# Kernel optimization log

Measured on AMD Instinct MI355X. Metric: run time of the kernel, lower is better.

Reference implementation:

```python
import jax, jax.numpy as jnp
import numpy as np

WIRES = 4
KS = 2
STRIDE = 2
OUT_CH = 4
LAYERS = 4
N_ROT = 8
SEED = 42
RATIO_IMPRIM = 0.3  # pennylane RandomLayers default


def _build_structure():
    # Mimics pennylane.templates.RandomLayers with a fixed seed: per layer, draw
    # random single-qubit rotations (RX/RY/RZ on random wires, consuming weights)
    # interleaved with random CNOTs at ratio_imprim.
    rng = np.random.RandomState(SEED)
    gates = []
    for l in range(LAYERS):
        i = 0
        while i < N_ROT:
            if rng.random_sample() > RATIO_IMPRIM:
                g = int(rng.randint(3))  # 0:RX 1:RY 2:RZ
                w = int(rng.randint(WIRES))
                gates.append(("R", g, w, l, i))
                i += 1
            else:
                cw, tw = rng.choice(WIRES, 2, replace=False)
                gates.append(("CNOT", int(cw), int(tw), 0, 0))
    return gates

GATES = _build_structure()


def _apply_1q(state, U, wire):
    # state: [P,2,2,2,2]; U: [2,2] shared or [P,2,2] per-patch
    ax = wire + 1
    s = jnp.moveaxis(state, ax, -1)
    if U.ndim == 2:
        s = jnp.einsum('ab,...b->...a', U, s)
    else:
        s = jnp.einsum('pab,p...b->p...a', U, s)
    return jnp.moveaxis(s, -1, ax)


def _apply_cnot(state, control, target):
    c_ax, t_ax = control + 1, target + 1
    s0 = jax.lax.index_in_dim(state, 0, c_ax, keepdims=False)
    s1 = jax.lax.index_in_dim(state, 1, c_ax, keepdims=False)
    t2 = t_ax - 1 if t_ax > c_ax else t_ax  # target axis after removing control axis
    return jnp.stack([s0, jnp.flip(s1, axis=t2)], axis=c_ax)


def _rot(g, t):
    h = t * 0.5
    c = jnp.cos(h)
    s = jnp.sin(h)
    z = jnp.zeros_like(c)
    if g == 0:    # RX
        U = jnp.stack([jnp.stack([c + 0j, -1j * s]), jnp.stack([-1j * s, c + 0j])])
    elif g == 1:  # RY
        U = jnp.stack([jnp.stack([c + 0j, -s + 0j]), jnp.stack([s + 0j, c + 0j])])
    else:         # RZ
        U = jnp.stack([jnp.stack([c - 1j * s, z + 0j]), jnp.stack([z + 0j, c + 1j * s])])
    return U.astype(jnp.complex64)


def _circuit(angles, weights):
    # angles: [P,4] RY encoding angles; returns [P, OUT_CH] PauliZ expvals
    P = angles.shape[0]
    state = jnp.zeros((P,) + (2,) * WIRES, jnp.complex64)
    state = state.at[(slice(None),) + (0,) * WIRES].set(1.0)
    for j in range(KS * KS):  # data-encoding RY, per-patch angle
        h = angles[:, j] * 0.5
        c, s = jnp.cos(h), jnp.sin(h)
        U = jnp.stack([jnp.stack([c, -s], -1), jnp.stack([s, c], -1)], -2).astype(jnp.complex64)
        state = _apply_1q(state, U, j)
    for kind, a, b, l, i in GATES:
        if kind == "R":
            state = _apply_1q(state, _rot(a, weights[l, i]), b)
        else:
            state = _apply_cnot(state, a, b)
    probs = (state.real ** 2 + state.imag ** 2).reshape(P, 2 ** WIRES)
    idx = np.arange(2 ** WIRES)
    signs = np.stack([1.0 - 2.0 * ((idx >> (WIRES - 1 - j)) & 1) for j in range(OUT_CH)])
    return probs @ jnp.asarray(signs, jnp.float32).T


def setup_inputs() -> dict:
    key = jax.random.key(0)
    k1, k2 = jax.random.split(key)
    img = jax.random.uniform(k1, (32, 512, 512, 3), dtype=jnp.float32)
    weights = jax.random.uniform(k2, (LAYERS, N_ROT), dtype=jnp.float32) * (2.0 * np.pi)
    return {"img": img, "weights": weights}


def reference(img, weights):
    bs, h, w, ch = img.shape
    x = img.mean(axis=-1) if ch > 1 else img[..., 0]  # [bs,h,w]
    h_out = (h - KS) // STRIDE + 1
    w_out = (w - KS) // STRIDE + 1
    # Faithful to original loop: patches only at j,k in range(0, h_out, stride),
    # written to out[j//kernel_size, k//kernel_size]; remaining entries stay zero.
    js = np.arange(0, h_out, STRIDE)
    ks_ = np.arange(0, w_out, STRIDE)
    ridx = js[:, None] + np.arange(KS)   # [nj,KS]
    cidx = ks_[:, None] + np.arange(KS)  # [nk,KS]
    patches = x[:, ridx]                 # [bs,nj,KS,w]
    patches = patches[:, :, :, cidx]     # [bs,nj,KS,nk,KS]
    patches = jnp.transpose(patches, (0, 1, 3, 2, 4)).reshape(-1, KS * KS)  # row-major like p.reshape(-1)
    res = _circuit(patches, weights)     # [P, OUT_CH]
    nj, nk = len(js), len(ks_)
    res = res.reshape(bs, nj, nk, OUT_CH).astype(jnp.float32)
    out = jnp.zeros((bs, h_out, w_out, OUT_CH), jnp.float32)
    out = out.at[:, js // KS[..., None] if False else (js // KS)[:, None], (ks_ // KS)[None, :], :].set(res)
    return out
```

## Files before the change

kernel.cpp:

```cpp
#include <hip/hip_runtime.h>
#include <cstdint>
#include <cstddef>

#define MAXG 128

namespace ct {

struct MT19937 {
  uint32_t mt[624] = {};
  int mti = 0;
  constexpr void seed(uint32_t s) {
    mt[0] = s;
    for (int i = 1; i < 624; i++)
      mt[i] = 1812433253u * (mt[i-1] ^ (mt[i-1] >> 30)) + (uint32_t)i;
    mti = 624;
  }
  constexpr uint32_t next() {
    if (mti >= 624) {
      for (int i = 0; i < 624; i++) {
        uint32_t y = (mt[i] & 0x80000000u) | (mt[(i+1) % 624] & 0x7fffffffu);
        mt[i] = mt[(i+397) % 624] ^ (y >> 1) ^ ((y & 1u) ? 2567483615u : 0u);
      }
      mti = 0;
    }
    uint32_t y = mt[mti++];
    y ^= y >> 11; y ^= (y << 7) & 2636928640u; y ^= (y << 15) & 4022730752u; y ^= y >> 18;
    return y;
  }
  constexpr double rdouble() {
    uint32_t a = next() >> 5, b = next() >> 6;
    return ((double)a * 67108864.0 + (double)b) / 9007199254740992.0;
  }
  constexpr uint32_t masked32(uint32_t rng, uint32_t mask) {
    uint32_t v = next() & mask;
    while (v > rng) v = next() & mask;
    return v;
  }
  constexpr uint32_t interval(uint32_t mx) {
    if (!mx) return 0;
    uint32_t mask = mx;
    mask |= mask >> 1; mask |= mask >> 2; mask |= mask >> 4; mask |= mask >> 8; mask |= mask >> 16;
    uint32_t v = next() & mask;
    while (v > mx) v = next() & mask;
    return v;
  }
};

struct CG { int n = 0; int code[MAXG] = {}; };

constexpr CG build_gates_ct() {
  CG gl{};
  MT19937 rng{};
  rng.seed(42);
  for (int l = 0; l < 4; l++) {
    int i = 0;
    while (i < 8) {
      if (rng.rdouble() > 0.3) {
        int g = (int)rng.masked32(2, 3);
        int w = (int)rng.masked32(3, 3);
        int widx = l * 8 + i;
        if (gl.n < MAXG) gl.code[gl.n++] = g | ((8 >> w) << 2) | (widx << 6);
        i++;
      } else {
        int perm[4] = {0, 1, 2, 3};
        for (int ii = 3; ii >= 1; ii--) {
          int j = (int)rng.interval((uint32_t)ii);
          int tmp = perm[ii]; perm[ii] = perm[j]; perm[j] = tmp;
        }
        int cw = perm[0], tw = perm[1];
        if (gl.n < MAXG) gl.code[gl.n++] = 3 | ((8 >> cw) << 2) | ((8 >> tw) << 6);
      }
    }
  }
  return gl;
}

constexpr CG GL = build_gates_ct();

}

template <int G>
__device__ __forceinline__ void apply_gates(float (&sr)[16], float (&si)[16],
                                            const float* __restrict__ w) {
  if constexpr (G < ct::GL.n) {
    constexpr int code = ct::GL.code[G];
    constexpr int kind = code & 3;
    if constexpr (kind == 3) {
      constexpr int cbit = (code >> 2) & 15, tbit = (code >> 6) & 15;
      float tr[16], ti[16];
      #pragma unroll
      for (int k = 0; k < 16; k++) {
        const int src = (k & cbit) ? (k ^ tbit) : k;
        tr[k] = sr[src]; ti[k] = si[src];
      }
      #pragma unroll
      for (int k = 0; k < 16; k++) { sr[k] = tr[k]; si[k] = ti[k]; }
    } else {
      constexpr int bit  = (code >> 2) & 15;
      constexpr int widx = (code >> 6) & 31;
      float sh, ch;
      __sincosf(0.5f * w[widx], &sh, &ch);
      float tr[16], ti[16];
      #pragma unroll
      for (int k = 0; k < 16; k++) {
        const int p = k ^ bit;
        if constexpr (kind == 0) {
          tr[k] = ch * sr[k] + sh * si[p];
          ti[k] = ch * si[k] - sh * sr[p];
        } else if constexpr (kind == 1) {
          if (k & bit) { tr[k] = ch * sr[k] + sh * sr[p]; ti[k] = ch * si[k] + sh * si[p]; }
          else         { tr[k] = ch * sr[k] - sh * sr[p]; ti[k] = ch * si[k] - sh * si[p]; }
        } else {
          if (k & bit) { tr[k] = ch * sr[k] - sh * si[k]; ti[k] = ch * si[k] + sh * sr[k]; }
          else         { tr[k] = ch * sr[k] + sh * si[k]; ti[k] = ch * si[k] - sh * sr[k]; }
        }
      }
      #pragma unroll
      for (int k = 0; k < 16; k++) { sr[k] = tr[k]; si[k] = ti[k]; }
    }
    apply_gates<G + 1>(sr, si, w);
  }
}

__global__ __launch_bounds__(64) void build_u(const float* __restrict__ w,
                                              float* __restrict__ ws) {
  const int c = threadIdx.x & 15;
  float sr[16], si[16];
  #pragma unroll
  for (int k = 0; k < 16; k++) { sr[k] = (k == c) ? 1.0f : 0.0f; si[k] = 0.0f; }

  apply_gates<0>(sr, si, w);

  if (threadIdx.x < 16) {
    float2* o = (float2*)ws;
    #pragma unroll
    for (int k = 0; k < 16; k++) o[k * 16 + c] = make_float2(sr[k], si[k]);
  }
}

__global__ __launch_bounds__(256) void qonv_main(const float* __restrict__ img,
                                                 const float* __restrict__ uws,
                                                 float* __restrict__ out) {
  __shared__ float4 U4[128];
  int t = threadIdx.x;
  if (t < 128) U4[t] = ((const float4*)uws)[t];
  __syncthreads();

  unsigned tid = blockIdx.x * 256u + (unsigned)t;
  int q  = tid & 63;
  int jj = (tid >> 6) & 127;
  int b  = tid >> 13;

  const float* row0 = img + (size_t)(b * 512 + 2 * jj) * 1536;
  const float* row1 = row0 + 1536;

  const float inv3 = 1.0f / 3.0f;
  float s16[2][16];
  #pragma unroll
  for (int p = 0; p < 2; p++) {
    int off = 384 * p + 6 * q;
    float2 x0 = *(const float2*)(row0 + off);
    float2 x1 = *(const float2*)(row0 + off + 2);
    float2 x2 = *(const float2*)(row0 + off + 4);
    float2 y0 = *(const float2*)(row1 + off);
    float2 y1 = *(const float2*)(row1 + off + 2);
    float2 y2 = *(const float2*)(row1 + off + 4);
    float a0 = (x0.x + x0.y + x1.x) * inv3;
    float a1 = (x1.y + x2.x + x2.y) * inv3;
    float a2 = (y0.x + y0.y + y1.x) * inv3;
    float a3 = (y1.y + y2.x + y2.y) * inv3;
    float c0, s0, c1, s1, c2, s2, c3, s3;
    __sincosf(0.5f * a0, &s0, &c0);
    __sincosf(0.5f * a1, &s1, &c1);
    __sincosf(0.5f * a2, &s2, &c2);
    __sincosf(0.5f * a3, &s3, &c3);
    float A[4] = {c0*c1, c0*s1, s0*c1, s0*s1};
    float B[4] = {c2*c3, c2*s3, s2*c3, s2*s3};
    #pragma unroll
    for (int hi = 0; hi < 4; hi++)
      #pragma unroll
      for (int lo = 0; lo < 4; lo++)
        s16[p][hi * 4 + lo] = A[hi] * B[lo];
  }

  float acc[2][4];
  #pragma unroll
  for (int p = 0; p < 2; p++)
    #pragma unroll
    for (int c = 0; c < 4; c++) acc[p][c] = 0.0f;

  #pragma unroll
  for (int k = 0; k < 16; k++) {
    float ar[2] = {0, 0}, ai[2] = {0, 0};
    #pragma unroll
    for (int i2 = 0; i2 < 8; i2++) {
      float4 u = U4[k * 8 + i2];
      #pragma unroll
      for (int p = 0; p < 2; p++) {
        ar[p] += u.x * s16[p][2*i2] + u.z * s16[p][2*i2+1];
        ai[p] += u.y * s16[p][2*i2] + u.w * s16[p][2*i2+1];
      }
    }
    #pragma unroll
    for (int p = 0; p < 2; p++) {
      float pk = ar[p]*ar[p] + ai[p]*ai[p];
      #pragma unroll
      for (int ch = 0; ch < 4; ch++) {
        if (k & (8 >> ch)) acc[p][ch] -= pk; else acc[p][ch] += pk;
      }
    }
  }

  float4* o = (float4*)out;
  size_t rowA = ((size_t)b * 256 + jj) * 256;
  size_t rowB = ((size_t)b * 256 + 128 + jj) * 256;
  const float4 z4 = make_float4(0.f, 0.f, 0.f, 0.f);
  o[rowA + q]       = make_float4(acc[0][0], acc[0][1], acc[0][2], acc[0][3]);
  o[rowA + 64 + q]  = make_float4(acc[1][0], acc[1][1], acc[1][2], acc[1][3]);
  o[rowA + 128 + q] = z4;
  o[rowA + 192 + q] = z4;
  o[rowB + q]       = z4;
  o[rowB + 64 + q]  = z4;
  o[rowB + 128 + q] = z4;
  o[rowB + 192 + q] = z4;
}

extern "C" void kernel_launch(void* const* d_in, const int* in_sizes, int n_in,
                              void* d_out, int out_size, void* d_ws, size_t ws_size,
                              hipStream_t stream) {
  const float* img = (const float*)d_in[0];
  const float* wts = (const float*)d_in[1];
  float* out = (float*)d_out;

  build_u<<<1, 64, 0, stream>>>(wts, (float*)d_ws);
  qonv_main<<<1024, 256, 0, stream>>>(img, (const float*)d_ws, out);
}
```

Baseline: 25.80 us.

## Move zero-fill into the unitary-build kernel and give each thread four patches

The first launch now uses 512 blocks. Block 0 builds the 16x16 circuit unitary, and the other blocks zero-fill the output regions that get no patch result. The main kernel no longer writes zeros. It now evaluates four patches per thread, covering two patch rows and two columns, with half as many blocks. The aim is to take the zero-store traffic off the compute kernel's critical path and to amortize the shared-memory unitary reads over more patches. The cost is higher register pressure and a strided fill loop that does div/mod index work.

```diff
diff --git a/kernel.cpp b/kernel.cpp
--- a/kernel.cpp
+++ b/kernel.cpp
@@ -122,19 +122,35 @@
   }
 }
 
-__global__ __launch_bounds__(64) void build_u(const float* __restrict__ w,
-                                              float* __restrict__ ws) {
-  const int c = threadIdx.x & 15;
-  float sr[16], si[16];
-  #pragma unroll
-  for (int k = 0; k < 16; k++) { sr[k] = (k == c) ? 1.0f : 0.0f; si[k] = 0.0f; }
-
-  apply_gates<0>(sr, si, w);
-
-  if (threadIdx.x < 16) {
-    float2* o = (float2*)ws;
-    #pragma unroll
-    for (int k = 0; k < 16; k++) o[k * 16 + c] = make_float2(sr[k], si[k]);
+__global__ __launch_bounds__(256) void build_u_fill(const float* __restrict__ w,
+                                                    float* __restrict__ ws,
+                                                    float* __restrict__ out) {
+  if (blockIdx.x == 0) {
+    if (threadIdx.x >= 64) return;
+    const int c = threadIdx.x & 15;
+    float sr[16], si[16];
+    #pragma unroll
+    for (int k = 0; k < 16; k++) { sr[k] = (k == c) ? 1.0f : 0.0f; si[k] = 0.0f; }
+    apply_gates<0>(sr, si, w);
+    if (threadIdx.x < 16) {
+      float2* o = (float2*)ws;
+      #pragma unroll
+      for (int k = 0; k < 16; k++) o[k * 16 + c] = make_float2(sr[k], si[k]);
+    }
+    return;
+  }
+  const unsigned PERB = 49152u;
+  const unsigned NZ   = PERB * 32u;
+  const unsigned stride = 511u * 256u;
+  float4* o4 = (float4*)out;
+  const float4 z = make_float4(0.f, 0.f, 0.f, 0.f);
+  for (unsigned zi = (blockIdx.x - 1) * 256u + threadIdx.x; zi < NZ; zi += stride) {
+    unsigned b = zi / PERB;
+    unsigned r = zi - b * PERB;
+    unsigned row, col;
+    if (r < 16384u) { row = r >> 7;          col = 128u + (r & 127u); }
+    else            { unsigned r2 = r - 16384u; row = 128u + (r2 >> 8); col = r2 & 255u; }
+    o4[((size_t)b * 256u + row) * 256u + col] = z;
   }
 }
 
@@ -148,61 +164,64 @@
 
   unsigned tid = blockIdx.x * 256u + (unsigned)t;
   int q  = tid & 63;
-  int jj = (tid >> 6) & 127;
-  int b  = tid >> 13;
-
-  const float* row0 = img + (size_t)(b * 512 + 2 * jj) * 1536;
-  const float* row1 = row0 + 1536;
+  int jj = (tid >> 6) & 63;
+  int b  = tid >> 12;
 
   const float inv3 = 1.0f / 3.0f;
-  float s16[2][16];
+  float s16[4][16];
   #pragma unroll
-  for (int p = 0; p < 2; p++) {
-    int off = 384 * p + 6 * q;
-    float2 x0 = *(const float2*)(row0 + off);
-    float2 x1 = *(const float2*)(row0 + off + 2);
-    float2 x2 = *(const float2*)(row0 + off + 4);
-    float2 y0 = *(const float2*)(row1 + off);
-    float2 y1 = *(const float2*)(row1 + off + 2);
-    float2 y2 = *(const float2*)(row1 + off + 4);
-    float a0 = (x0.x + x0.y + x1.x) * inv3;
-    float a1 = (x1.y + x2.x + x2.y) * inv3;
-    float a2 = (y0.x + y0.y + y1.x) * inv3;
-    float a3 = (y1.y + y2.x + y2.y) * inv3;
-    float c0, s0, c1, s1, c2, s2, c3, s3;
-    __sincosf(0.5f * a0, &s0, &c0);
-    __sincosf(0.5f * a1, &s1, &c1);
-    __sincosf(0.5f * a2, &s2, &c2);
-    __sincosf(0.5f * a3, &s3, &c3);
-    float A[4] = {c0*c1, c0*s1, s0*c1, s0*s1};
-    float B[4] = {c2*c3, c2*s3, s2*c3, s2*s3};
-    #pragma unroll
-    for (int hi = 0; hi < 4; hi++)
-      #pragma unroll
-      for (int lo = 0; lo < 4; lo++)
-        s16[p][hi * 4 + lo] = A[hi] * B[lo];
-  }
-
-  float acc[2][4];
+  for (int pr = 0; pr < 2; pr++) {
+    const float* row0 = img + (size_t)(b * 512 + 2 * jj + 128 * pr) * 1536;
+    const float* row1 = row0 + 1536;
+    #pragma unroll
+    for (int pc = 0; pc < 2; pc++) {
+      const int p = pr * 2 + pc;
+      int off = 384 * pc + 6 * q;
+      float2 x0 = *(const float2*)(row0 + off);
+      float2 x1 = *(const float2*)(row0 + off + 2);
+      float2 x2 = *(const float2*)(row0 + off + 4);
+      float2 y0 = *(const float2*)(row1 + off);
+      float2 y1 = *(const float2*)(row1 + off + 2);
+      float2 y2 = *(const float2*)(row1 + off + 4);
+      float a0 = (x0.x + x0.y + x1.x) * inv3;
+      float a1 = (x1.y + x2.x + x2.y) * inv3;
+      float a2 = (y0.x + y0.y + y1.x) * inv3;
+      float a3 = (y1.y + y2.x + y2.y) * inv3;
+      float c0, s0, c1, s1, c2, s2, c3, s3;
+      __sincosf(0.5f * a0, &s0, &c0);
+      __sincosf(0.5f * a1, &s1, &c1);
+      __sincosf(0.5f * a2, &s2, &c2);
+      __sincosf(0.5f * a3, &s3, &c3);
+      float A[4] = {c0*c1, c0*s1, s0*c1, s0*s1};
+      float B[4] = {c2*c3, c2*s3, s2*c3, s2*s3};
+      #pragma unroll
+      for (int hi = 0; hi < 4; hi++)
+        #pragma unroll
+        for (int lo = 0; lo < 4; lo++)
+          s16[p][hi * 4 + lo] = A[hi] * B[lo];
+    }
+  }
+
+  float acc[4][4];
   #pragma unroll
-  for (int p = 0; p < 2; p++)
+  for (int p = 0; p < 4; p++)
     #pragma unroll
     for (int c = 0; c < 4; c++) acc[p][c] = 0.0f;
 
   #pragma unroll
   for (int k = 0; k < 16; k++) {
-    float ar[2] = {0, 0}, ai[2] = {0, 0};
+    float ar[4] = {0, 0, 0, 0}, ai[4] = {0, 0, 0, 0};
     #pragma unroll
     for (int i2 = 0; i2 < 8; i2++) {
       float4 u = U4[k * 8 + i2];
       #pragma unroll
-      for (int p = 0; p < 2; p++) {
+      for (int p = 0; p < 4; p++) {
         ar[p] += u.x * s16[p][2*i2] + u.z * s16[p][2*i2+1];
         ai[p] += u.y * s16[p][2*i2] + u.w * s16[p][2*i2+1];
       }
     }
     #pragma unroll
-    for (int p = 0; p < 2; p++) {
+    for (int p = 0; p < 4; p++) {
       float pk = ar[p]*ar[p] + ai[p]*ai[p];
       #pragma unroll
       for (int ch = 0; ch < 4; ch++) {
@@ -213,16 +232,11 @@
 
   float4* o = (float4*)out;
   size_t rowA = ((size_t)b * 256 + jj) * 256;
-  size_t rowB = ((size_t)b * 256 + 128 + jj) * 256;
-  const float4 z4 = make_float4(0.f, 0.f, 0.f, 0.f);
-  o[rowA + q]       = make_float4(acc[0][0], acc[0][1], acc[0][2], acc[0][3]);
-  o[rowA + 64 + q]  = make_float4(acc[1][0], acc[1][1], acc[1][2], acc[1][3]);
-  o[rowA + 128 + q] = z4;
-  o[rowA + 192 + q] = z4;
-  o[rowB + q]       = z4;
-  o[rowB + 64 + q]  = z4;
-  o[rowB + 128 + q] = z4;
-  o[rowB + 192 + q] = z4;
+  size_t rowB = ((size_t)b * 256 + 64 + jj) * 256;
+  o[rowA + q]      = make_float4(acc[0][0], acc[0][1], acc[0][2], acc[0][3]);
+  o[rowA + 64 + q] = make_float4(acc[1][0], acc[1][1], acc[1][2], acc[1][3]);
+  o[rowB + q]      = make_float4(acc[2][0], acc[2][1], acc[2][2], acc[2][3]);
+  o[rowB + 64 + q] = make_float4(acc[3][0], acc[3][1], acc[3][2], acc[3][3]);
 }
 
 extern "C" void kernel_launch(void* const* d_in, const int* in_sizes, int n_in,
@@ -232,6 +246,6 @@
   const float* wts = (const float*)d_in[1];
   float* out = (float*)d_out;
 
-  build_u<<<1, 64, 0, stream>>>(wts, (float*)d_ws);
-  qonv_main<<<1024, 256, 0, stream>>>(img, (const float*)d_ws, out);
-}
+  build_u_fill<<<512, 256, 0, stream>>>(wts, (float*)d_ws, out);
+  qonv_main<<<512, 256, 0, stream>>>(img, (const float*)d_ws, out);
+}
```

Result: slower. 27.84 us (+7.9%).

## Fuse unitary construction into main kernel and issue zero stores early

Applied to the files above, without the earlier changes.

Removes the separate single-block build_u launch. Each block now has 16 threads rebuild the 16x16 circuit unitary directly into shared memory, so the extra launch and its workspace round trip go away. The zero-fill stores are issued before the image loads so they overlap with the gate simulation and sincos work. Sincos now uses the hardware sin/cos builtins with a pre-scaled argument. The cost is redundant unitary construction in every block, serialized on one partial wave before the barrier.

```diff
diff --git a/kernel.cpp b/kernel.cpp
--- a/kernel.cpp
+++ b/kernel.cpp
@@ -79,6 +79,12 @@
 
 }
 
+__device__ __forceinline__ void half_sincos(float a, float& s, float& c) {
+  const float r = a * 0.07957747154594767f;
+  s = __builtin_amdgcn_sinf(r);
+  c = __builtin_amdgcn_cosf(r);
+}
+
 template <int G>
 __device__ __forceinline__ void apply_gates(float (&sr)[16], float (&si)[16],
                                             const float* __restrict__ w) {
@@ -99,7 +105,7 @@
       constexpr int bit  = (code >> 2) & 15;
       constexpr int widx = (code >> 6) & 31;
       float sh, ch;
-      __sincosf(0.5f * w[widx], &sh, &ch);
+      half_sincos(w[widx], sh, ch);
       float tr[16], ti[16];
       #pragma unroll
       for (int k = 0; k < 16; k++) {
@@ -122,38 +128,43 @@
   }
 }
 
-__global__ __launch_bounds__(64) void build_u(const float* __restrict__ w,
-                                              float* __restrict__ ws) {
-  const int c = threadIdx.x & 15;
-  float sr[16], si[16];
-  #pragma unroll
-  for (int k = 0; k < 16; k++) { sr[k] = (k == c) ? 1.0f : 0.0f; si[k] = 0.0f; }
-
-  apply_gates<0>(sr, si, w);
-
-  if (threadIdx.x < 16) {
-    float2* o = (float2*)ws;
-    #pragma unroll
-    for (int k = 0; k < 16; k++) o[k * 16 + c] = make_float2(sr[k], si[k]);
-  }
-}
-
-__global__ __launch_bounds__(256) void qonv_main(const float* __restrict__ img,
-                                                 const float* __restrict__ uws,
-                                                 float* __restrict__ out) {
+__global__ __launch_bounds__(256) void qonv_fused(const float* __restrict__ img,
+                                                  const float* __restrict__ wts,
+                                                  float* __restrict__ out) {
   __shared__ float4 U4[128];
-  int t = threadIdx.x;
-  if (t < 128) U4[t] = ((const float4*)uws)[t];
-  __syncthreads();
-
-  unsigned tid = blockIdx.x * 256u + (unsigned)t;
-  int q  = tid & 63;
-  int jj = (tid >> 6) & 127;
-  int b  = tid >> 13;
+  const int t = threadIdx.x;
+
+  if (t < 16) {
+    const int c = t;
+    float sr[16], si[16];
+    #pragma unroll
+    for (int k = 0; k < 16; k++) { sr[k] = (k == c) ? 1.0f : 0.0f; si[k] = 0.0f; }
+    apply_gates<0>(sr, si, wts);
+    float2* uo = (float2*)U4;
+    #pragma unroll
+    for (int k = 0; k < 16; k++) uo[k * 16 + c] = make_float2(sr[k], si[k]);
+  }
+
+  const unsigned tid = blockIdx.x * 256u + (unsigned)t;
+  const int q  = tid & 63;
+  const int jj = (tid >> 6) & 127;
+  const int b  = tid >> 13;
+
+  float4* o = (float4*)out;
+  size_t rowA = ((size_t)b * 256 + jj) * 256;
+  size_t rowB = ((size_t)b * 256 + 128 + jj) * 256;
+  {
+    const float4 z4 = make_float4(0.f, 0.f, 0.f, 0.f);
+    o[rowA + 128 + q] = z4;
+    o[rowA + 192 + q] = z4;
+    o[rowB + q]       = z4;
+    o[rowB + 64 + q]  = z4;
+    o[rowB + 128 + q] = z4;
+    o[rowB + 192 + q] = z4;
+  }
 
   const float* row0 = img + (size_t)(b * 512 + 2 * jj) * 1536;
   const float* row1 = row0 + 1536;
-
   const float inv3 = 1.0f / 3.0f;
   float s16[2][16];
   #pragma unroll
@@ -170,10 +181,10 @@
     float a2 = (y0.x + y0.y + y1.x) * inv3;
     float a3 = (y1.y + y2.x + y2.y) * inv3;
     float c0, s0, c1, s1, c2, s2, c3, s3;
-    __sincosf(0.5f * a0, &s0, &c0);
-    __sincosf(0.5f * a1, &s1, &c1);
-    __sincosf(0.5f * a2, &s2, &c2);
-    __sincosf(0.5f * a3, &s3, &c3);
+    half_sincos(a0, s0, c0);
+    half_sincos(a1, s1, c1);
+    half_sincos(a2, s2, c2);
+    half_sincos(a3, s3, c3);
     float A[4] = {c0*c1, c0*s1, s0*c1, s0*s1};
     float B[4] = {c2*c3, c2*s3, s2*c3, s2*s3};
     #pragma unroll
@@ -189,6 +200,8 @@
     #pragma unroll
     for (int c = 0; c < 4; c++) acc[p][c] = 0.0f;
 
+  __syncthreads();
+
   #pragma unroll
   for (int k = 0; k < 16; k++) {
     float ar[2] = {0, 0}, ai[2] = {0, 0};
@@ -211,18 +224,8 @@
     }
   }
 
-  float4* o = (float4*)out;
-  size_t rowA = ((size_t)b * 256 + jj) * 256;
-  size_t rowB = ((size_t)b * 256 + 128 + jj) * 256;
-  const float4 z4 = make_float4(0.f, 0.f, 0.f, 0.f);
-  o[rowA + q]       = make_float4(acc[0][0], acc[0][1], acc[0][2], acc[0][3]);
-  o[rowA + 64 + q]  = make_float4(acc[1][0], acc[1][1], acc[1][2], acc[1][3]);
-  o[rowA + 128 + q] = z4;
-  o[rowA + 192 + q] = z4;
-  o[rowB + q]       = z4;
-  o[rowB + 64 + q]  = z4;
-  o[rowB + 128 + q] = z4;
-  o[rowB + 192 + q] = z4;
+  o[rowA + q]      = make_float4(acc[0][0], acc[0][1], acc[0][2], acc[0][3]);
+  o[rowA + 64 + q] = make_float4(acc[1][0], acc[1][1], acc[1][2], acc[1][3]);
 }
 
 extern "C" void kernel_launch(void* const* d_in, const int* in_sizes, int n_in,
@@ -232,6 +235,5 @@
   const float* wts = (const float*)d_in[1];
   float* out = (float*)d_out;
 
-  build_u<<<1, 64, 0, stream>>>(wts, (float*)d_ws);
-  qonv_main<<<1024, 256, 0, stream>>>(img, (const float*)d_ws, out);
-}
+  qonv_fused<<<1024, 256, 0, stream>>>(img, wts, out);
+}
```

Result: faster. 23.97 us (-7.1%).
